# Kernel tuning notes

Hardware: AMD Instinct MI355X
Metric: run time of the kernel (lower is better)

The kernel has to match this reference:

```python
import jax, jax.numpy as jnp
import numpy as np

N = 100000        # nodes
E = 1600000       # edges (avg degree 16)
D_IN = 128        # input_dim
HID = 128         # hidden
L = 2             # num_layers
EPS = 1e-5        # LayerNorm eps (torch default)


def setup_inputs() -> dict:
    key = jax.random.key(0)
    ks = jax.random.split(key, 5)
    x = jax.random.normal(ks[0], (N, D_IN), dtype=jnp.float32)
    edge_index = jax.random.randint(ks[1], (2, E), 0, N, dtype=jnp.int64)
    e_feat = jax.random.uniform(ks[2], (E,), dtype=jnp.float32)
    # nn.Linear(input_dim, hidden): weight [hidden, input_dim], bias [hidden]
    lin_w = jax.random.normal(ks[3], (HID, D_IN), dtype=jnp.float32) / np.float32(np.sqrt(D_IN))
    lin_b = jax.random.normal(ks[4], (HID,), dtype=jnp.float32) * 0.01
    ln_scale = jnp.ones((L, HID), dtype=jnp.float32)
    ln_bias = jnp.zeros((L, HID), dtype=jnp.float32)
    return {"x": x, "edge_index": edge_index, "e_feat": e_feat,
            "lin_w": lin_w, "lin_b": lin_b,
            "ln_scale": ln_scale, "ln_bias": ln_bias}


def _layernorm(h, scale, bias):
    mu = jnp.mean(h, axis=-1, keepdims=True)
    var = jnp.mean(jnp.square(h - mu), axis=-1, keepdims=True)
    return (h - mu) * jax.lax.rsqrt(var + EPS) * scale + bias


def reference(x, edge_index, e_feat, lin_w, lin_b, ln_scale, ln_bias):
    src, dst = edge_index[0], edge_index[1]
    h = x @ lin_w.T + lin_b            # [N, HID]
    ori = h
    for i in range(L):
        if i != 0:                      # res=True
            h = h + ori
        h = _layernorm(h, ln_scale[i], ln_bias[i])   # norm=True
        h = jax.nn.relu(h)              # relu=True; dp=0 -> dropout no-op
        # GraphConv(weight=False, bias=False): weighted SpMM aggregation
        msg = h[src] * e_feat[:, None]  # [E, HID]
        h = jax.ops.segment_sum(msg, dst, num_segments=N)  # [N, HID]
    return h
```

## Files before the change

### kernel.cpp

```cpp
#include <hip/hip_runtime.h>
#include <hip/hip_fp16.h>


constexpr int N_NODES = 100000;
constexpr int N_EDGES = 1600000;
constexpr int HID     = 128;
constexpr int NBKT    = (N_NODES + 511) / 512;
constexpr int BCAP    = 9216;
constexpr int BSTRIDE = 12800;
constexpr float LN_EPS = 1e-5f;

typedef __attribute__((ext_vector_type(8))) short short8;
typedef __attribute__((ext_vector_type(4))) float floatx4;
typedef __attribute__((ext_vector_type(2))) float f32x2;

__device__ inline unsigned pack_bf16x2(float a, float b) {
    unsigned ua = __float_as_uint(a), ub = __float_as_uint(b);
    ua += 0x7fff + ((ua >> 16) & 1);
    ub += 0x7fff + ((ub >> 16) & 1);
    return (ua >> 16) | (ub & 0xffff0000u);
}
__device__ inline float bflo(unsigned u) { return __uint_as_float(u << 16); }
__device__ inline float bfhi(unsigned u) { return __uint_as_float(u & 0xffff0000u); }

__global__ __launch_bounds__(256) void k_bin(const int* __restrict__ ei,
                                             const float* __restrict__ ef,
                                             int* __restrict__ gcur,
                                             int* __restrict__ gbufDst,
                                             unsigned* __restrict__ gbufRec) {
    __shared__ int cnt[NBKT];
    __shared__ int incl[256];
    __shared__ int gbase[NBKT];
    __shared__ int sdst[2048];
    __shared__ unsigned ssw[2048];
    const int t = threadIdx.x;

    for (int e0 = blockIdx.x * 2048; e0 < N_EDGES; e0 += gridDim.x * 2048) {
        for (int i = t; i < NBKT; i += 256) cnt[i] = 0;
        __syncthreads();

        const int nE = min(2048, N_EDGES - e0);
        int ed[8], ep[8]; unsigned er[8];
        const int base = e0 + t * 8;
        if (base + 8 <= N_EDGES) {
            int4 s0 = *(const int4*)&ei[base];
            int4 s1 = *(const int4*)&ei[base + 4];
            int4 d0 = *(const int4*)&ei[N_EDGES + base];
            int4 d1 = *(const int4*)&ei[N_EDGES + base + 4];
            float4 w0 = *(const float4*)&ef[base];
            float4 w1 = *(const float4*)&ef[base + 4];
            int es[8]; float ew[8];
            es[0]=s0.x; es[1]=s0.y; es[2]=s0.z; es[3]=s0.w;
            es[4]=s1.x; es[5]=s1.y; es[6]=s1.z; es[7]=s1.w;
            ed[0]=d0.x; ed[1]=d0.y; ed[2]=d0.z; ed[3]=d0.w;
            ed[4]=d1.x; ed[5]=d1.y; ed[6]=d1.z; ed[7]=d1.w;
            ew[0]=w0.x; ew[1]=w0.y; ew[2]=w0.z; ew[3]=w0.w;
            ew[4]=w1.x; ew[5]=w1.y; ew[6]=w1.z; ew[7]=w1.w;
#pragma unroll
            for (int k = 0; k < 8; ++k) {
                unsigned q = __float2uint_rn(ew[k] * 32768.0f);
                if (q > 32767u) q = 32767u;
                er[k] = (q << 17) | (unsigned)es[k];
                ep[k] = atomicAdd(&cnt[ed[k] >> 9], 1);
            }
        } else {
#pragma unroll
            for (int k = 0; k < 8; ++k) {
                int idx = base + k;
                if (idx < N_EDGES) {
                    int s = ei[idx]; ed[k] = ei[N_EDGES + idx];
                    unsigned q = __float2uint_rn(ef[idx] * 32768.0f);
                    if (q > 32767u) q = 32767u;
                    er[k] = (q << 17) | (unsigned)s;
                    ep[k] = atomicAdd(&cnt[ed[k] >> 9], 1);
                } else ed[k] = -1;
            }
        }
        __syncthreads();

        int v = (t < NBKT) ? cnt[t] : 0;
        incl[t] = v;
        for (int o = 1; o < 256; o <<= 1) {
            __syncthreads();
            int u = (t >= o) ? incl[t - o] : 0;
            __syncthreads();
            incl[t] += u;
        }
        __syncthreads();
        if (t < NBKT) gbase[t] = atomicAdd(&gcur[t], v);
        __syncthreads();

#pragma unroll
        for (int k = 0; k < 8; ++k) {
            if (ed[k] < 0) continue;
            int b = ed[k] >> 9;
            int idx = incl[b] - cnt[b] + ep[k];
            sdst[idx] = ed[k];
            ssw[idx]  = er[k];
        }
        __syncthreads();

        for (int j = t; j < nE; j += 256) {
            int d = sdst[j];
            int b = d >> 9;
            int pos = gbase[b] + (j - (incl[b] - cnt[b]));
            if (pos < BCAP) {
                gbufDst[(size_t)b * BCAP + pos] = d;
                gbufRec[(size_t)b * BCAP + pos] = ssw[j];
            }
        }
        __syncthreads();
    }
}

__global__ __launch_bounds__(512) void k_build(const int* __restrict__ gcur,
                                               const int* __restrict__ gbufDst,
                                               const unsigned* __restrict__ gbufRec,
                                               unsigned* __restrict__ rowinfo,
                                               unsigned* __restrict__ rec) {
    __shared__ int cnt[512];
    __shared__ int cur[512];
    __shared__ unsigned sorted[BSTRIDE];
    const int t     = threadIdx.x;
    const int b     = blockIdx.x;
    const int nbase = b * 512;
    const int nb    = min(gcur[b], BCAP);
    const unsigned cb = (unsigned)b * (unsigned)BSTRIDE;

    cnt[t] = 0;
    for (int i = t; i < BSTRIDE; i += 512) sorted[i] = 0;
    __syncthreads();

    const int*      bd = gbufDst + (size_t)b * BCAP;
    const unsigned* bs = gbufRec + (size_t)b * BCAP;

    for (int i = t; i < nb; i += 512) atomicAdd(&cnt[bd[i] - nbase], 1);
    __syncthreads();

    const int deg = cnt[t];
    int v = (deg + 7) & ~7;
    cur[t] = v;
    for (int o = 1; o < 512; o <<= 1) {
        __syncthreads();
        int u = (t >= o) ? cur[t - o] : 0;
        __syncthreads();
        cur[t] += u;
    }
    __syncthreads();
    const int padTotal = cur[511];
    const int excl = cur[t] - v;
    __syncthreads();
    cur[t] = excl;
    if (nbase + t < N_NODES)
        rowinfo[nbase + t] = ((cb + (unsigned)excl) << 10) | (unsigned)deg;
    __syncthreads();

    for (int i = t; i < nb; i += 512) {
        int d = bd[i];
        int pos = atomicAdd(&cur[d - nbase], 1);
        sorted[pos] = bs[i];
    }
    __syncthreads();
    for (int i = t; i < padTotal; i += 512) rec[(size_t)cb + i] = sorted[i];
}

__global__ __launch_bounds__(256) void k_gemm_mfma(const float* __restrict__ x,
                                                   const float* __restrict__ W,
                                                   const float* __restrict__ bias,
                                                   const float* __restrict__ lns,
                                                   const float* __restrict__ lnb,
                                                   unsigned* __restrict__ orib,
                                                   unsigned* __restrict__ hact) {
    __shared__ __align__(16) char smem[128 * 136 * 2 + 64 * 136 * 2];
    ushort (*Ws)[136] = (ushort(*)[136])smem;
    ushort (*Xs)[136] = (ushort(*)[136])(smem + 128 * 136 * 2);
    float  (*Hs)[132] = (float(*)[132])smem;

    const int t    = threadIdx.x;
    const int row0 = blockIdx.x * 64;

    {
        const float4* Wf = (const float4*)W;
#pragma unroll
        for (int i = 0; i < 8; ++i) {
            int g = t + 256 * i;
            float4 p = Wf[g * 2], q = Wf[g * 2 + 1];
            uint4 vv = make_uint4(pack_bf16x2(p.x, p.y), pack_bf16x2(p.z, p.w),
                                  pack_bf16x2(q.x, q.y), pack_bf16x2(q.z, q.w));
            int r = g >> 4;
            int c = (g & 15) * 8;
            *(uint4*)&Ws[r][c] = vv;
        }
    }
    {
        const float4* xg = (const float4*)x;
        const int base = blockIdx.x * 2048;
#pragma unroll
        for (int i = 0; i < 8; ++i) {
            int f = t + 256 * i;
            int g = base + f;
            float4 vv = make_float4(0.f, 0.f, 0.f, 0.f);
            if (g < N_NODES * 32) vv = xg[g];
            int r = f >> 5;
            int c = (f & 31) * 4;
            uint2 p = make_uint2(pack_bf16x2(vv.x, vv.y), pack_bf16x2(vv.z, vv.w));
            *(uint2*)&Xs[r][c] = p;
        }
    }
    __syncthreads();

    const int wv   = t >> 6;
    const int l    = t & 63;
    const int mrow = l & 15;
    const int kq   = l >> 4;

    floatx4 acc[8];
#pragma unroll
    for (int i = 0; i < 8; ++i) acc[i] = (floatx4){0.f, 0.f, 0.f, 0.f};

#pragma unroll
    for (int ks = 0; ks < 4; ++ks) {
        short8 a = *(const short8*)&Xs[wv * 16 + mrow][ks * 32 + kq * 8];
#pragma unroll
        for (int tc = 0; tc < 8; ++tc) {
            short8 bb = *(const short8*)&Ws[tc * 16 + mrow][ks * 32 + kq * 8];
            acc[tc] = __builtin_amdgcn_mfma_f32_16x16x32_bf16(a, bb, acc[tc], 0, 0, 0);
        }
    }
    __syncthreads();

#pragma unroll
    for (int tc = 0; tc < 8; ++tc)
#pragma unroll
        for (int r = 0; r < 4; ++r)
            Hs[wv * 16 + kq * 4 + r][tc * 16 + mrow] = acc[tc][r];
    __syncthreads();

    const float2 b2  = ((const float2*)bias)[l];
    const float2 sc2 = ((const float2*)lns)[l];
    const float2 bb2 = ((const float2*)lnb)[l];
    for (int rr = 0; rr < 16; ++rr) {
        const int lrow = wv * 16 + rr;
        const int grow = row0 + lrow;
        if (grow >= N_NODES) break;
        float2 vv = *(const float2*)&Hs[lrow][l * 2];
        vv.x += b2.x; vv.y += b2.y;
        orib[(size_t)grow * 64 + l] = pack_bf16x2(vv.x, vv.y);
        float s  = vv.x + vv.y;
        float s2 = vv.x * vv.x + vv.y * vv.y;
#pragma unroll
        for (int m = 1; m < 64; m <<= 1) {
            s  += __shfl_xor(s, m);
            s2 += __shfl_xor(s2, m);
        }
        const float mu   = s * (1.0f / 128.0f);
        const float var  = s2 * (1.0f / 128.0f) - mu * mu;
        const float rstd = rsqrtf(var + LN_EPS);
        float y0 = fmaxf((vv.x - mu) * rstd * sc2.x + bb2.x, 0.0f);
        float y1 = fmaxf((vv.y - mu) * rstd * sc2.y + bb2.y, 0.0f);
        hact[(size_t)(l >> 3) * (size_t)(N_NODES * 8) + (size_t)grow * 8 + (l & 7)] =
            pack_bf16x2(y0, y1);
    }
}

template <int MODE>
__global__ __launch_bounds__(256) void k_spmm(const unsigned* __restrict__ rowinfo,
                                              const unsigned* __restrict__ rec,
                                              const unsigned* __restrict__ Hb,
                                              unsigned* __restrict__ agg,
                                              float* __restrict__ out) {
    const int slice = blockIdx.x & 7;
    const int nb    = blockIdx.x >> 3;
    const int wv    = threadIdx.x >> 6;
    const int lane  = threadIdx.x & 63;
    const int sub   = lane >> 3;
    const int col   = lane & 7;
    const int node0 = nb * 32 + wv * 8;

    const unsigned* __restrict__ Hs = Hb + (size_t)slice * (size_t)(N_NODES * 8) + col;

    const unsigned vinfo = rowinfo[node0 + (lane & 7)];

    int beg, pd;
    unsigned cr0, cr1, cr2;
    {
        unsigned info = __shfl(vinfo, 0);
        beg = (int)(info >> 10);
        int deg = (int)(info & 1023u);
        pd = (deg + 7) & ~7;
        cr0 = (sub < pd)      ? rec[beg + sub]      : 0u;
        cr1 = (8  + sub < pd) ? rec[beg + 8 + sub]  : 0u;
        cr2 = (16 + sub < pd) ? rec[beg + 16 + sub] : 0u;
    }

#pragma unroll
    for (int m = 0; m < 8; ++m) {
        const int cbeg = beg, cpd = pd;
        unsigned nr0 = 0u, nr1 = 0u, nr2 = 0u;
        if (m < 7) {
            unsigned info = __shfl(vinfo, m + 1);
            beg = (int)(info >> 10);
            int deg = (int)(info & 1023u);
            pd = (deg + 7) & ~7;
            nr0 = (sub < pd)      ? rec[beg + sub]      : 0u;
            nr1 = (8  + sub < pd) ? rec[beg + 8 + sub]  : 0u;
            nr2 = (16 + sub < pd) ? rec[beg + 16 + sub] : 0u;
        }

        unsigned v0 = Hs[(size_t)(cr0 & 0x1FFFFu) * 8u];
        unsigned v1 = Hs[(size_t)(cr1 & 0x1FFFFu) * 8u];
        unsigned v2 = Hs[(size_t)(cr2 & 0x1FFFFu) * 8u];
        float w0 = (float)(cr0 >> 17), w1 = (float)(cr1 >> 17), w2 = (float)(cr2 >> 17);
        float ax = w0 * bflo(v0), ay = w0 * bfhi(v0);
        ax = fmaf(w1, bflo(v1), ax); ay = fmaf(w1, bfhi(v1), ay);
        ax = fmaf(w2, bflo(v2), ax); ay = fmaf(w2, bfhi(v2), ay);

        for (int e = 24; e < cpd; e += 8) {
            unsigned r = (e + sub < cpd) ? rec[cbeg + e + sub] : 0u;
            unsigned v = Hs[(size_t)(r & 0x1FFFFu) * 8u];
            float w = (float)(r >> 17);
            ax = fmaf(w, bflo(v), ax); ay = fmaf(w, bfhi(v), ay);
        }

        ax += __shfl_xor(ax, 8);  ay += __shfl_xor(ay, 8);
        ax += __shfl_xor(ax, 16); ay += __shfl_xor(ay, 16);
        ax += __shfl_xor(ax, 32); ay += __shfl_xor(ay, 32);
        ax *= 3.0517578125e-05f;
        ay *= 3.0517578125e-05f;

        if (sub == 0) {
            const int node = node0 + m;
            if (MODE == 0) {
                unsigned u = (unsigned)__half_as_ushort(__float2half(ax)) |
                             ((unsigned)__half_as_ushort(__float2half(ay)) << 16);
                __builtin_nontemporal_store(u, agg + (size_t)node * 64 + slice * 8 + col);
            } else {
                f32x2 o2 = {ax, ay};
                __builtin_nontemporal_store(o2, (f32x2*)out + (size_t)node * 64 + slice * 8 + col);
            }
        }
        cr0 = nr0; cr1 = nr1; cr2 = nr2;
    }
}

__global__ __launch_bounds__(256) void k_ln(const unsigned* __restrict__ agg,
                                            const unsigned* __restrict__ orib,
                                            const float* __restrict__ lns,
                                            const float* __restrict__ lnb,
                                            unsigned* __restrict__ hact2) {
    const int wid  = (blockIdx.x * 256 + threadIdx.x) >> 6;
    const int lane = threadIdx.x & 63;
    unsigned a = agg[(size_t)wid * 64 + lane];
    unsigned o = orib[(size_t)wid * 64 + lane];
    float vx = __half2float(__ushort_as_half((unsigned short)(a & 0xffffu))) + bflo(o);
    float vy = __half2float(__ushort_as_half((unsigned short)(a >> 16)))     + bfhi(o);
    float s  = vx + vy;
    float s2 = vx * vx + vy * vy;
#pragma unroll
    for (int m = 1; m < 64; m <<= 1) {
        s  += __shfl_xor(s, m);
        s2 += __shfl_xor(s2, m);
    }
    const float mu   = s * (1.0f / 128.0f);
    const float var  = s2 * (1.0f / 128.0f) - mu * mu;
    const float rstd = rsqrtf(var + LN_EPS);
    const float2 sc = ((const float2*)lns)[lane];
    const float2 bb = ((const float2*)lnb)[lane];
    float y0 = fmaxf((vx - mu) * rstd * sc.x + bb.x, 0.0f);
    float y1 = fmaxf((vy - mu) * rstd * sc.y + bb.y, 0.0f);
    hact2[(size_t)(lane >> 3) * (size_t)(N_NODES * 8) + (size_t)wid * 8 + (lane & 7)] =
        pack_bf16x2(y0, y1);
}

extern "C" void kernel_launch(void* const* d_in, const int* in_sizes, int n_in,
                              void* d_out, int out_size, void* d_ws, size_t ws_size,
                              hipStream_t stream) {
    const float* x   = (const float*)d_in[0];
    const int*   ei  = (const int*)d_in[1];
    const float* ef  = (const float*)d_in[2];
    const float* W   = (const float*)d_in[3];
    const float* b   = (const float*)d_in[4];
    const float* lns = (const float*)d_in[5];
    const float* lnb = (const float*)d_in[6];
    float* out = (float*)d_out;

    unsigned* orib = (unsigned*)d_out;
    unsigned* agg  = (unsigned*)d_out + (size_t)N_NODES * 64;

    unsigned* rec     = (unsigned*)d_ws;
    unsigned* hact    = rec + (size_t)NBKT * BSTRIDE;
    unsigned* hact2   = hact + (size_t)N_NODES * 64;
    unsigned* gbufRec = hact2 + (size_t)N_NODES * 64;
    int*      gcur    = (int*)(gbufRec + (size_t)NBKT * BCAP);
    unsigned* rowinfo = (unsigned*)(gcur + NBKT);
    int*      gbufDst = (int*)(rowinfo + N_NODES);

    hipMemsetAsync(gcur, 0, NBKT * sizeof(int), stream);
    k_bin<<<782, 256, 0, stream>>>(ei, ef, gcur, gbufDst, gbufRec);
    k_build<<<NBKT, 512, 0, stream>>>(gcur, gbufDst, gbufRec, rowinfo, rec);

    k_gemm_mfma<<<(N_NODES + 63) / 64, 256, 0, stream>>>(x, W, b, lns, lnb, orib, hact);

    k_spmm<0><<<25000, 256, 0, stream>>>(rowinfo, rec, hact, agg, nullptr);
    k_ln<<<25000, 256, 0, stream>>>(agg, orib, lns + HID, lnb + HID, hact2);
    k_spmm<1><<<25000, 256, 0, stream>>>(rowinfo, rec, hact2, nullptr, out);
}
```

Measured before the change: 384.4 us.

## Switch activations and edge weights to fp16 with packed half2 FMA aggregation

Replaces bf16 storage of activations and the 15-bit fixed-point edge weight with fp16 throughout. The GEMM now uses f16 MFMA, and the SpMM inner loop accumulates with packed __hfma2 on half2 pairs instead of scalar fp32 FMAs. Per-node edge lists are padded to at least 24 zero entries, so the per-load bounds predicates can be dropped. This cuts ALU work and branches in the gather loop. In exchange, accumulation happens in fp16, which risks precision loss and overflow, and the larger bucket stride with clamping could silently drop edges if a bucket overflows.

```diff
diff --git a/kernel.cpp b/kernel.cpp
--- a/kernel.cpp
+++ b/kernel.cpp
@@ -7,21 +7,20 @@
 constexpr int HID     = 128;
 constexpr int NBKT    = (N_NODES + 511) / 512;
 constexpr int BCAP    = 9216;
-constexpr int BSTRIDE = 12800;
+constexpr int BSTRIDE = 15360;
 constexpr float LN_EPS = 1e-5f;
 
-typedef __attribute__((ext_vector_type(8))) short short8;
+typedef __attribute__((ext_vector_type(8))) _Float16 half8;
 typedef __attribute__((ext_vector_type(4))) float floatx4;
 typedef __attribute__((ext_vector_type(2))) float f32x2;
 
-__device__ inline unsigned pack_bf16x2(float a, float b) {
-    unsigned ua = __float_as_uint(a), ub = __float_as_uint(b);
-    ua += 0x7fff + ((ua >> 16) & 1);
-    ub += 0x7fff + ((ub >> 16) & 1);
-    return (ua >> 16) | (ub & 0xffff0000u);
-}
-__device__ inline float bflo(unsigned u) { return __uint_as_float(u << 16); }
-__device__ inline float bfhi(unsigned u) { return __uint_as_float(u & 0xffff0000u); }
+union U32H2 { unsigned u; __half2 h; };
+
+__device__ inline unsigned packh2(float a, float b) {
+    U32H2 c; c.h = __floats2half2_rn(a, b); return c.u;
+}
+__device__ inline float f16lo(unsigned u) { U32H2 c; c.u = u; return __low2float(c.h); }
+__device__ inline float f16hi(unsigned u) { U32H2 c; c.u = u; return __high2float(c.h); }
 
 __global__ __launch_bounds__(256) void k_bin(const int* __restrict__ ei,
                                              const float* __restrict__ ef,
@@ -58,9 +57,8 @@
             ew[4]=w1.x; ew[5]=w1.y; ew[6]=w1.z; ew[7]=w1.w;
 #pragma unroll
             for (int k = 0; k < 8; ++k) {
-                unsigned q = __float2uint_rn(ew[k] * 32768.0f);
-                if (q > 32767u) q = 32767u;
-                er[k] = (q << 17) | (unsigned)es[k];
+                unsigned hw = (unsigned)__half_as_ushort(__float2half_rn(ew[k]));
+                er[k] = (hw << 17) | (unsigned)es[k];
                 ep[k] = atomicAdd(&cnt[ed[k] >> 9], 1);
             }
         } else {
@@ -69,9 +67,8 @@
                 int idx = base + k;
                 if (idx < N_EDGES) {
                     int s = ei[idx]; ed[k] = ei[N_EDGES + idx];
-                    unsigned q = __float2uint_rn(ef[idx] * 32768.0f);
-                    if (q > 32767u) q = 32767u;
-                    er[k] = (q << 17) | (unsigned)s;
+                    unsigned hw = (unsigned)__half_as_ushort(__float2half_rn(ef[idx]));
+                    er[k] = (hw << 17) | (unsigned)s;
                     ep[k] = atomicAdd(&cnt[ed[k] >> 9], 1);
                 } else ed[k] = -1;
             }
@@ -139,6 +136,7 @@
 
     const int deg = cnt[t];
     int v = (deg + 7) & ~7;
+    if (v < 24) v = 24;
     cur[t] = v;
     for (int o = 1; o < 512; o <<= 1) {
         __syncthreads();
@@ -147,18 +145,18 @@
         cur[t] += u;
     }
     __syncthreads();
-    const int padTotal = cur[511];
+    const int padTotal = min(cur[511], BSTRIDE);
     const int excl = cur[t] - v;
     __syncthreads();
     cur[t] = excl;
     if (nbase + t < N_NODES)
-        rowinfo[nbase + t] = ((cb + (unsigned)excl) << 10) | (unsigned)deg;
+        rowinfo[nbase + t] = ((cb + (unsigned)excl) << 10) | (unsigned)v;
     __syncthreads();
 
     for (int i = t; i < nb; i += 512) {
         int d = bd[i];
         int pos = atomicAdd(&cur[d - nbase], 1);
-        sorted[pos] = bs[i];
+        if (pos < BSTRIDE) sorted[pos] = bs[i];
     }
     __syncthreads();
     for (int i = t; i < padTotal; i += 512) rec[(size_t)cb + i] = sorted[i];
@@ -185,8 +183,8 @@
         for (int i = 0; i < 8; ++i) {
             int g = t + 256 * i;
             float4 p = Wf[g * 2], q = Wf[g * 2 + 1];
-            uint4 vv = make_uint4(pack_bf16x2(p.x, p.y), pack_bf16x2(p.z, p.w),
-                                  pack_bf16x2(q.x, q.y), pack_bf16x2(q.z, q.w));
+            uint4 vv = make_uint4(packh2(p.x, p.y), packh2(p.z, p.w),
+                                  packh2(q.x, q.y), packh2(q.z, q.w));
             int r = g >> 4;
             int c = (g & 15) * 8;
             *(uint4*)&Ws[r][c] = vv;
@@ -203,7 +201,7 @@
             if (g < N_NODES * 32) vv = xg[g];
             int r = f >> 5;
             int c = (f & 31) * 4;
-            uint2 p = make_uint2(pack_bf16x2(vv.x, vv.y), pack_bf16x2(vv.z, vv.w));
+            uint2 p = make_uint2(packh2(vv.x, vv.y), packh2(vv.z, vv.w));
             *(uint2*)&Xs[r][c] = p;
         }
     }
@@ -220,11 +218,11 @@
 
 #pragma unroll
     for (int ks = 0; ks < 4; ++ks) {
-        short8 a = *(const short8*)&Xs[wv * 16 + mrow][ks * 32 + kq * 8];
+        half8 a = *(const half8*)&Xs[wv * 16 + mrow][ks * 32 + kq * 8];
 #pragma unroll
         for (int tc = 0; tc < 8; ++tc) {
-            short8 bb = *(const short8*)&Ws[tc * 16 + mrow][ks * 32 + kq * 8];
-            acc[tc] = __builtin_amdgcn_mfma_f32_16x16x32_bf16(a, bb, acc[tc], 0, 0, 0);
+            half8 bb = *(const half8*)&Ws[tc * 16 + mrow][ks * 32 + kq * 8];
+            acc[tc] = __builtin_amdgcn_mfma_f32_16x16x32_f16(a, bb, acc[tc], 0, 0, 0);
         }
     }
     __syncthreads();
@@ -245,7 +243,7 @@
         if (grow >= N_NODES) break;
         float2 vv = *(const float2*)&Hs[lrow][l * 2];
         vv.x += b2.x; vv.y += b2.y;
-        orib[(size_t)grow * 64 + l] = pack_bf16x2(vv.x, vv.y);
+        orib[(size_t)grow * 64 + l] = packh2(vv.x, vv.y);
         float s  = vv.x + vv.y;
         float s2 = vv.x * vv.x + vv.y * vv.y;
 #pragma unroll
@@ -259,7 +257,7 @@
         float y0 = fmaxf((vv.x - mu) * rstd * sc2.x + bb2.x, 0.0f);
         float y1 = fmaxf((vv.y - mu) * rstd * sc2.y + bb2.y, 0.0f);
         hact[(size_t)(l >> 3) * (size_t)(N_NODES * 8) + (size_t)grow * 8 + (l & 7)] =
-            pack_bf16x2(y0, y1);
+            packh2(y0, y1);
     }
 }
 
@@ -277,7 +275,8 @@
     const int col   = lane & 7;
     const int node0 = nb * 32 + wv * 8;
 
-    const unsigned* __restrict__ Hs = Hb + (size_t)slice * (size_t)(N_NODES * 8) + col;
+    const unsigned* __restrict__ Hu = Hb + (size_t)slice * (size_t)(N_NODES * 8);
+    const unsigned ucol = (unsigned)col;
 
     const unsigned vinfo = rowinfo[node0 + (lane & 7)];
 
@@ -286,11 +285,9 @@
     {
         unsigned info = __shfl(vinfo, 0);
         beg = (int)(info >> 10);
-        int deg = (int)(info & 1023u);
-        pd = (deg + 7) & ~7;
-        cr0 = (sub < pd)      ? rec[beg + sub]      : 0u;
-        cr1 = (8  + sub < pd) ? rec[beg + 8 + sub]  : 0u;
-        cr2 = (16 + sub < pd) ? rec[beg + 16 + sub] : 0u;
+        pd  = (int)(info & 1023u);
+        const unsigned* ra = rec + beg + sub;
+        cr0 = ra[0]; cr1 = ra[8]; cr2 = ra[16];
     }
 
 #pragma unroll
@@ -300,40 +297,45 @@
         if (m < 7) {
             unsigned info = __shfl(vinfo, m + 1);
             beg = (int)(info >> 10);
-            int deg = (int)(info & 1023u);
-            pd = (deg + 7) & ~7;
-            nr0 = (sub < pd)      ? rec[beg + sub]      : 0u;
-            nr1 = (8  + sub < pd) ? rec[beg + 8 + sub]  : 0u;
-            nr2 = (16 + sub < pd) ? rec[beg + 16 + sub] : 0u;
-        }
-
-        unsigned v0 = Hs[(size_t)(cr0 & 0x1FFFFu) * 8u];
-        unsigned v1 = Hs[(size_t)(cr1 & 0x1FFFFu) * 8u];
-        unsigned v2 = Hs[(size_t)(cr2 & 0x1FFFFu) * 8u];
-        float w0 = (float)(cr0 >> 17), w1 = (float)(cr1 >> 17), w2 = (float)(cr2 >> 17);
-        float ax = w0 * bflo(v0), ay = w0 * bfhi(v0);
-        ax = fmaf(w1, bflo(v1), ax); ay = fmaf(w1, bfhi(v1), ay);
-        ax = fmaf(w2, bflo(v2), ax); ay = fmaf(w2, bfhi(v2), ay);
+            pd  = (int)(info & 1023u);
+            const unsigned* ra = rec + beg + sub;
+            nr0 = ra[0]; nr1 = ra[8]; nr2 = ra[16];
+        }
+
+        unsigned v0 = Hu[((cr0 & 0x1FFFFu) << 3) + ucol];
+        unsigned v1 = Hu[((cr1 & 0x1FFFFu) << 3) + ucol];
+        unsigned v2 = Hu[((cr2 & 0x1FFFFu) << 3) + ucol];
+
+        U32H2 a; a.u = 0u;
+        {
+            U32H2 hv, hw;
+            hv.u = v0; hw.u = __builtin_amdgcn_perm(cr0 >> 1, cr0 >> 1, 0x07060706u);
+            a.h = __hfma2(hv.h, hw.h, a.h);
+            hv.u = v1; hw.u = __builtin_amdgcn_perm(cr1 >> 1, cr1 >> 1, 0x07060706u);
+            a.h = __hfma2(hv.h, hw.h, a.h);
+            hv.u = v2; hw.u = __builtin_amdgcn_perm(cr2 >> 1, cr2 >> 1, 0x07060706u);
+            a.h = __hfma2(hv.h, hw.h, a.h);
+        }
 
         for (int e = 24; e < cpd; e += 8) {
-            unsigned r = (e + sub < cpd) ? rec[cbeg + e + sub] : 0u;
-            unsigned v = Hs[(size_t)(r & 0x1FFFFu) * 8u];
-            float w = (float)(r >> 17);
-            ax = fmaf(w, bflo(v), ax); ay = fmaf(w, bfhi(v), ay);
-        }
-
+            unsigned r = rec[cbeg + e + sub];
+            unsigned v = Hu[((r & 0x1FFFFu) << 3) + ucol];
+            U32H2 hv, hw;
+            hv.u = v; hw.u = __builtin_amdgcn_perm(r >> 1, r >> 1, 0x07060706u);
+            a.h = __hfma2(hv.h, hw.h, a.h);
+        }
+
+        float2 f = __half22float2(a.h);
+        float ax = f.x, ay = f.y;
         ax += __shfl_xor(ax, 8);  ay += __shfl_xor(ay, 8);
         ax += __shfl_xor(ax, 16); ay += __shfl_xor(ay, 16);
         ax += __shfl_xor(ax, 32); ay += __shfl_xor(ay, 32);
-        ax *= 3.0517578125e-05f;
-        ay *= 3.0517578125e-05f;
 
         if (sub == 0) {
             const int node = node0 + m;
             if (MODE == 0) {
-                unsigned u = (unsigned)__half_as_ushort(__float2half(ax)) |
-                             ((unsigned)__half_as_ushort(__float2half(ay)) << 16);
-                __builtin_nontemporal_store(u, agg + (size_t)node * 64 + slice * 8 + col);
+                __builtin_nontemporal_store(packh2(ax, ay),
+                                            agg + (size_t)node * 64 + slice * 8 + col);
             } else {
                 f32x2 o2 = {ax, ay};
                 __builtin_nontemporal_store(o2, (f32x2*)out + (size_t)node * 64 + slice * 8 + col);
@@ -352,8 +354,8 @@
     const int lane = threadIdx.x & 63;
     unsigned a = agg[(size_t)wid * 64 + lane];
     unsigned o = orib[(size_t)wid * 64 + lane];
-    float vx = __half2float(__ushort_as_half((unsigned short)(a & 0xffffu))) + bflo(o);
-    float vy = __half2float(__ushort_as_half((unsigned short)(a >> 16)))     + bfhi(o);
+    float vx = f16lo(a) + f16lo(o);
+    float vy = f16hi(a) + f16hi(o);
     float s  = vx + vy;
     float s2 = vx * vx + vy * vy;
 #pragma unroll
@@ -369,7 +371,7 @@
     float y0 = fmaxf((vx - mu) * rstd * sc.x + bb.x, 0.0f);
     float y1 = fmaxf((vy - mu) * rstd * sc.y + bb.y, 0.0f);
     hact2[(size_t)(lane >> 3) * (size_t)(N_NODES * 8) + (size_t)wid * 8 + (lane & 7)] =
-        pack_bf16x2(y0, y1);
+        packh2(y0, y1);
 }
 
 extern "C" void kernel_launch(void* const* d_in, const int* in_sizes, int n_in,
```

New measurement: 394.2 us. +2.6%, slower.
